# Performance work log

Hardware: AMD Instinct MI355X
Metric: run time of the kernel (lower is better)

Reference implementation:

```python
import jax, jax.numpy as jnp
import numpy as np


def _gcn_conv(x, edge_index, edge_weight, W, b, n_nodes):
    # PyG GCNConv with normalize=True: add self-loops (weight 1), symmetric norm,
    # transform then aggregate: out[col] += norm * (x @ W)[row], plus bias.
    row = jnp.concatenate([edge_index[0], jnp.arange(n_nodes)])
    col = jnp.concatenate([edge_index[1], jnp.arange(n_nodes)])
    w = jnp.concatenate([edge_weight, jnp.ones((n_nodes,), x.dtype)])
    deg = jax.ops.segment_sum(w, col, num_segments=n_nodes)
    dinv = jnp.where(deg > 0, jax.lax.rsqrt(jnp.maximum(deg, 1e-12)), 0.0)
    norm = dinv[row] * w * dinv[col]            # [E+N]
    h = x @ W                                   # [N, out]
    msg = h[row] * norm[:, None]                # [E+N, out]
    out = jax.ops.segment_sum(msg, col, num_segments=n_nodes)
    return out + b


def setup_inputs() -> dict:
    key = jax.random.key(0)
    ks = jax.random.split(key, 6)
    N, E, F_IN, H, C = 50000, 800000, 512, 128, 40
    features = jax.random.normal(ks[0], (N, F_IN), jnp.float32)
    edge_index = jax.random.randint(ks[1], (2, E), 0, N, jnp.int64)
    edge_weight = jax.random.uniform(ks[2], (E,), jnp.float32)
    W1 = jax.random.normal(ks[3], (F_IN, H), jnp.float32) * 0.05
    b1 = jnp.zeros((H,), jnp.float32)
    W2 = jax.random.normal(ks[4], (H, C), jnp.float32) * 0.05
    b2 = jnp.zeros((C,), jnp.float32)
    return {"features": features, "edge_index": edge_index, "edge_weight": edge_weight,
            "W1": W1, "b1": b1, "W2": W2, "b2": b2}


def reference(features, edge_index, edge_weight, W1, b1, W2, b2):
    n_nodes = features.shape[0]
    x = _gcn_conv(features, edge_index, edge_weight, W1, b1, n_nodes)
    x = jax.nn.relu(x)
    # F.dropout(training=self.training): identity in eval mode
    x = _gcn_conv(x, edge_index, edge_weight, W2, b2, n_nodes)
    return jax.nn.log_softmax(x, axis=1)
```

## Files before the change

kernel.cpp:

```cpp
#include <hip/hip_runtime.h>
#include <math.h>

#define FIN  512
#define HDIM 128
#define CDIM 40
#define CPAD 48
#define CAP  64

typedef __attribute__((ext_vector_type(8))) short shortx8;
typedef __attribute__((ext_vector_type(4))) float f32x4;
typedef __attribute__((ext_vector_type(2))) float floatx2;

__device__ inline unsigned short f2bf(float x) {
    unsigned u = __builtin_bit_cast(unsigned, x);
    unsigned r = u + 0x7fffu + ((u >> 16) & 1u);
    return (unsigned short)(r >> 16);
}
__device__ inline float bfu(unsigned short v) { return __builtin_bit_cast(float, (unsigned)v << 16); }
__device__ inline float bfhi(unsigned u) { return __builtin_bit_cast(float, u & 0xffff0000u); }
__device__ inline unsigned char f2fp8(float x) {
    return (unsigned char)(__builtin_amdgcn_cvt_pk_fp8_f32(x, x, 0, false) & 0xff);
}
__device__ inline floatx2 fp8x2_dec(unsigned short v) {
    return __builtin_amdgcn_cvt_pk_f32_fp8((int)(unsigned)v, false);
}
__device__ inline int cur_cnt(unsigned long long p) { return min((int)(p >> 40), CAP); }
__device__ inline float cur_dinv(unsigned long long p) {
    return rsqrtf(1.0f + (float)(p & ((1ULL << 40) - 1)) * 2.3283064365386963e-10f);
}

#define PREPB 280
__global__ void k_fill(const int* __restrict__ row, const int* __restrict__ col,
                       const float* __restrict__ w,
                       unsigned long long* __restrict__ cursor,
                       unsigned* __restrict__ bkt, int E, int eblocks,
                       const float* __restrict__ W1, const float* __restrict__ W2,
                       unsigned short* __restrict__ W1T, unsigned short* __restrict__ W2T) {
    if ((int)blockIdx.x >= eblocks) {
        const int i = ((int)blockIdx.x - eblocks) * 256 + (int)threadIdx.x;
        if (i < FIN * HDIM) {
            const int k = i >> 7, nn = i & 127;
            W1T[nn * FIN + k] = f2bf(W1[i]);
        } else {
            const int j = i - FIN * HDIM;
            const int nn = j >> 7, k = j & 127;
            W2T[j] = (nn < CDIM) ? f2bf(W2[k * CDIM + nn]) : (unsigned short)0;
        }
        return;
    }
    const int e = blockIdx.x * blockDim.x + threadIdx.x;
    if (e >= E) return;
    const int c = col[e];
    const float we = w[e];
    const unsigned long long wfix = (unsigned long long)(we * 4294967296.0f);
    const unsigned long long old = atomicAdd(&cursor[c], (1ULL << 40) | wfix);
    const int p = (int)(old >> 40);
    const unsigned wb = (__builtin_bit_cast(unsigned, we) + 0x8000u) >> 16;
    if (p < CAP) bkt[(size_t)c * CAP + p] = (wb << 16) | (unsigned)row[e];
}

#define G1_LDA 72
__global__ __launch_bounds__(256) void k_gemm1(const float* __restrict__ A,
                                               const unsigned short* __restrict__ W1T,
                                               const unsigned long long* __restrict__ cursor,
                                               unsigned char* __restrict__ h1f8, int M) {
    __shared__ short As[128 * G1_LDA];
    __shared__ short Bs[128 * G1_LDA];
    const int tid  = threadIdx.x;
    const int wave = tid >> 6;
    const int lane = tid & 63;
    const int quad = lane >> 4;
    const int mr   = lane & 15;
    const int m0w  = (wave & 1) * 64;
    const int n0w  = (wave >> 1) * 64;
    const int m0b  = blockIdx.x * 128;

    const int srow = tid >> 1;
    const int spart = tid & 1;

    f32x4 acc[4][4];
#pragma unroll
    for (int i = 0; i < 4; i++)
#pragma unroll
        for (int j = 0; j < 4; j++) acc[i][j] = (f32x4)0.f;

    const int grow = m0b + srow;
    const bool arow_ok = grow < M;
    const float* ap = A + (size_t)grow * FIN + spart * 32;
    const unsigned short* bp = W1T + (size_t)srow * FIN + spart * 32;

    for (int k0 = 0; k0 < FIN; k0 += 64) {
#pragma unroll
        for (int i = 0; i < 4; i++) {
            float4 v0 = make_float4(0.f, 0.f, 0.f, 0.f), v1 = v0;
            if (arow_ok) {
                v0 = *(const float4*)(ap + k0 + i * 8);
                v1 = *(const float4*)(ap + k0 + i * 8 + 4);
            }
            shortx8 pk;
            pk[0] = (short)f2bf(v0.x); pk[1] = (short)f2bf(v0.y);
            pk[2] = (short)f2bf(v0.z); pk[3] = (short)f2bf(v0.w);
            pk[4] = (short)f2bf(v1.x); pk[5] = (short)f2bf(v1.y);
            pk[6] = (short)f2bf(v1.z); pk[7] = (short)f2bf(v1.w);
            *(shortx8*)&As[srow * G1_LDA + spart * 32 + i * 8] = pk;
        }
#pragma unroll
        for (int i = 0; i < 4; i++)
            *(shortx8*)&Bs[srow * G1_LDA + spart * 32 + i * 8] =
                *(const shortx8*)(bp + k0 + i * 8);
        __syncthreads();

#pragma unroll
        for (int kk = 0; kk < 2; kk++) {
            shortx8 af[4], bfr[4];
#pragma unroll
            for (int mt = 0; mt < 4; mt++)
                af[mt] = *(shortx8*)&As[(m0w + mt * 16 + mr) * G1_LDA + kk * 32 + quad * 8];
#pragma unroll
            for (int nt = 0; nt < 4; nt++)
                bfr[nt] = *(shortx8*)&Bs[(n0w + nt * 16 + mr) * G1_LDA + kk * 32 + quad * 8];
#pragma unroll
            for (int mt = 0; mt < 4; mt++)
#pragma unroll
                for (int nt = 0; nt < 4; nt++)
                    acc[mt][nt] = __builtin_amdgcn_mfma_f32_16x16x32_bf16(
                        af[mt], bfr[nt], acc[mt][nt], 0, 0, 0);
        }
        __syncthreads();
    }
#pragma unroll
    for (int mt = 0; mt < 4; mt++)
#pragma unroll
        for (int r = 0; r < 4; r++) {
            const int om = m0b + m0w + mt * 16 + quad * 4 + r;
            if (om < M) {
                const float dv = cur_dinv(cursor[om]);
#pragma unroll
                for (int nt = 0; nt < 4; nt++)
                    h1f8[(size_t)om * HDIM + n0w + nt * 16 + mr] = f2fp8(dv * acc[mt][nt][r]);
            }
        }
}

#define W2LD 130
__global__ __launch_bounds__(256) void k_g1g2(
    const unsigned long long* __restrict__ cursor, const unsigned* __restrict__ bkt,
    const unsigned char* __restrict__ h1f8,
    const float* __restrict__ b1,
    const unsigned short* __restrict__ W2T,
    unsigned short* __restrict__ h2, int n_nodes) {
    __shared__ unsigned short W2s[CPAD * W2LD];
    __shared__ unsigned short Xs[4 * 128];
    const int tid  = threadIdx.x;
    const int wave = tid >> 6;
    const int lane = tid & 63;
    const int loff = lane * 2;

    for (int i = tid; i < CPAD * (HDIM / 8); i += 256) {
        const int r = i >> 4, j = (i & 15) * 8;
        *(shortx8*)&W2s[r * W2LD + j] = *(const shortx8*)(W2T + r * HDIM + j);
    }
    __syncthreads();

    const int node = blockIdx.x * 4 + wave;
    if (node >= n_nodes) return;
    const unsigned long long cp = cursor[node];
    const int cnt = cur_cnt(cp);
    const float dl = cur_dinv(cp);
    const char* bb = (const char*)bkt + (unsigned)node * (CAP * 4u);
    float a0 = 0.f, a1 = 0.f, c0 = 0.f, c1 = 0.f;
    int s = 0;
    for (; s + 8 <= cnt; s += 8) {
        const uint4 qa = *(const uint4*)(bb + (unsigned)s * 4u);
        const uint4 qb = *(const uint4*)(bb + (unsigned)s * 4u + 16u);
        const unsigned o0 = (qa.x & 0xffffu) * 128u + (unsigned)loff;
        const unsigned o1 = (qa.y & 0xffffu) * 128u + (unsigned)loff;
        const unsigned o2 = (qa.z & 0xffffu) * 128u + (unsigned)loff;
        const unsigned o3 = (qa.w & 0xffffu) * 128u + (unsigned)loff;
        const unsigned o4 = (qb.x & 0xffffu) * 128u + (unsigned)loff;
        const unsigned o5 = (qb.y & 0xffffu) * 128u + (unsigned)loff;
        const unsigned o6 = (qb.z & 0xffffu) * 128u + (unsigned)loff;
        const unsigned o7 = (qb.w & 0xffffu) * 128u + (unsigned)loff;
        const unsigned short v0 = *(const unsigned short*)(h1f8 + o0);
        const unsigned short v1 = *(const unsigned short*)(h1f8 + o1);
        const unsigned short v2 = *(const unsigned short*)(h1f8 + o2);
        const unsigned short v3 = *(const unsigned short*)(h1f8 + o3);
        const unsigned short v4 = *(const unsigned short*)(h1f8 + o4);
        const unsigned short v5 = *(const unsigned short*)(h1f8 + o5);
        const unsigned short v6 = *(const unsigned short*)(h1f8 + o6);
        const unsigned short v7 = *(const unsigned short*)(h1f8 + o7);
        const floatx2 f0 = fp8x2_dec(v0), f1 = fp8x2_dec(v1), f2 = fp8x2_dec(v2), f3 = fp8x2_dec(v3);
        const floatx2 f4 = fp8x2_dec(v4), f5 = fp8x2_dec(v5), f6 = fp8x2_dec(v6), f7 = fp8x2_dec(v7);
        a0 += bfhi(qa.x) * f0.x + bfhi(qa.y) * f1.x + bfhi(qa.z) * f2.x + bfhi(qa.w) * f3.x;
        a1 += bfhi(qa.x) * f0.y + bfhi(qa.y) * f1.y + bfhi(qa.z) * f2.y + bfhi(qa.w) * f3.y;
        c0 += bfhi(qb.x) * f4.x + bfhi(qb.y) * f5.x + bfhi(qb.z) * f6.x + bfhi(qb.w) * f7.x;
        c1 += bfhi(qb.x) * f4.y + bfhi(qb.y) * f5.y + bfhi(qb.z) * f6.y + bfhi(qb.w) * f7.y;
    }
    for (; s + 4 <= cnt; s += 4) {
        const uint4 qa = *(const uint4*)(bb + (unsigned)s * 4u);
        const unsigned o0 = (qa.x & 0xffffu) * 128u + (unsigned)loff;
        const unsigned o1 = (qa.y & 0xffffu) * 128u + (unsigned)loff;
        const unsigned o2 = (qa.z & 0xffffu) * 128u + (unsigned)loff;
        const unsigned o3 = (qa.w & 0xffffu) * 128u + (unsigned)loff;
        const unsigned short v0 = *(const unsigned short*)(h1f8 + o0);
        const unsigned short v1 = *(const unsigned short*)(h1f8 + o1);
        const unsigned short v2 = *(const unsigned short*)(h1f8 + o2);
        const unsigned short v3 = *(const unsigned short*)(h1f8 + o3);
        const floatx2 f0 = fp8x2_dec(v0), f1 = fp8x2_dec(v1), f2 = fp8x2_dec(v2), f3 = fp8x2_dec(v3);
        a0 += bfhi(qa.x) * f0.x + bfhi(qa.y) * f1.x + bfhi(qa.z) * f2.x + bfhi(qa.w) * f3.x;
        a1 += bfhi(qa.x) * f0.y + bfhi(qa.y) * f1.y + bfhi(qa.z) * f2.y + bfhi(qa.w) * f3.y;
    }
    for (; s < cnt; s++) {
        const unsigned p = *(const unsigned*)(bb + (unsigned)s * 4u);
        const unsigned short v = *(const unsigned short*)(h1f8 + (p & 0xffffu) * 128u + (unsigned)loff);
        const floatx2 f = fp8x2_dec(v);
        a0 += bfhi(p) * f.x;
        a1 += bfhi(p) * f.y;
    }
    a0 += c0; a1 += c1;
    const unsigned short vs = *(const unsigned short*)(h1f8 + (unsigned)node * 128u + (unsigned)loff);
    const floatx2 fs = fp8x2_dec(vs);
    a0 = fmaxf(dl * (a0 + fs.x) + b1[loff], 0.f);
    a1 = fmaxf(dl * (a1 + fs.y) + b1[loff + 1], 0.f);
    *(unsigned*)&Xs[wave * 128 + loff] = (unsigned)f2bf(a0) | ((unsigned)f2bf(a1) << 16);

    const int quad = lane >> 4;
    const int mr   = lane & 15;
    f32x4 acc2[3];
#pragma unroll
    for (int nt = 0; nt < 3; nt++) acc2[nt] = (f32x4)0.f;
#pragma unroll
    for (int kc = 0; kc < 4; kc++) {
        shortx8 af = (shortx8)0;
        if (mr == 0) af = *(const shortx8*)&Xs[wave * 128 + kc * 32 + quad * 8];
#pragma unroll
        for (int nt = 0; nt < 3; nt++) {
            const shortx8 bfr = *(const shortx8*)&W2s[(nt * 16 + mr) * W2LD + kc * 32 + quad * 8];
            acc2[nt] = __builtin_amdgcn_mfma_f32_16x16x32_bf16(af, bfr, acc2[nt], 0, 0, 0);
        }
    }
    if (lane < 16) {
        h2[(size_t)node * 32 + lane]      = f2bf(dl * acc2[0][0]);
        h2[(size_t)node * 32 + 16 + lane] = f2bf(dl * acc2[1][0]);
        if (lane < 8)
            h2[(size_t)n_nodes * 32 + (size_t)node * 8 + lane] = f2bf(dl * acc2[2][0]);
    }
}

__global__ __launch_bounds__(256) void k_gather2(
    const unsigned long long* __restrict__ cursor, const unsigned* __restrict__ bkt,
    const unsigned short* __restrict__ h2,
    const float* __restrict__ b2,
    float* __restrict__ out, int n_nodes) {
    const int node = blockIdx.x * 4 + (threadIdx.x >> 6);
    const int lane = threadIdx.x & 63;
    if (node >= n_nodes) return;
    const bool act = lane < CDIM;
    const unsigned long long cp = cursor[node];
    const int cnt = cur_cnt(cp);
    const float dl = cur_dinv(cp);
    const char* bb = (const char*)bkt + (unsigned)node * (CAP * 4u);
    const char* h2c = (const char*)h2;
    const unsigned strB = (lane < 32) ? 64u : 16u;
    const unsigned cb   = (lane < 32) ? (unsigned)lane * 2u
                                      : (unsigned)n_nodes * 64u + (unsigned)(lane - 32) * 2u;
    float acc = 0.f, accb = 0.f;
    int s = 0;
    for (; s + 4 <= cnt; s += 4) {
        const uint4 q = *(const uint4*)(bb + (unsigned)s * 4u);
        if (act) {
            const unsigned short u0 = *(const unsigned short*)(h2c + (q.x & 0xffffu) * strB + cb);
            const unsigned short u1 = *(const unsigned short*)(h2c + (q.y & 0xffffu) * strB + cb);
            const unsigned short u2 = *(const unsigned short*)(h2c + (q.z & 0xffffu) * strB + cb);
            const unsigned short u3 = *(const unsigned short*)(h2c + (q.w & 0xffffu) * strB + cb);
            acc  += bfhi(q.x) * bfu(u0) + bfhi(q.y) * bfu(u1);
            accb += bfhi(q.z) * bfu(u2) + bfhi(q.w) * bfu(u3);
        }
    }
    for (; s < cnt; s++) {
        const unsigned p = *(const unsigned*)(bb + (unsigned)s * 4u);
        if (act) acc += bfhi(p) * bfu(*(const unsigned short*)(h2c + (p & 0xffffu) * strB + cb));
    }
    acc += accb;
    if (act) {
        const unsigned short us = *(const unsigned short*)(h2c + (unsigned)node * strB + cb);
        acc = dl * (acc + bfu(us)) + b2[lane];
    }
    float m = act ? acc : -INFINITY;
#pragma unroll
    for (int off = 32; off; off >>= 1) m = fmaxf(m, __shfl_xor(m, off));
    float se = act ? expf(acc - m) : 0.f;
#pragma unroll
    for (int off = 32; off; off >>= 1) se += __shfl_xor(se, off);
    if (act) out[(size_t)node * CDIM + lane] = acc - m - logf(se);
}

extern "C" void kernel_launch(void* const* d_in, const int* in_sizes, int n_in,
                              void* d_out, int out_size, void* d_ws, size_t ws_size,
                              hipStream_t stream) {
    const float* features = (const float*)d_in[0];
    const int*   eidx     = (const int*)d_in[1];
    const float* ew       = (const float*)d_in[2];
    const float* W1       = (const float*)d_in[3];
    const float* b1       = (const float*)d_in[4];
    const float* W2       = (const float*)d_in[5];
    const float* b2       = (const float*)d_in[6];
    float* out = (float*)d_out;

    const int Nn = in_sizes[0] / FIN;
    const int E  = in_sizes[2];
    const int* row = eidx;
    const int* col = eidx + E;

    char* ws = (char*)d_ws;
    size_t off = 0;
    auto alloc = [&](size_t bytes) { void* p = ws + off; off += (bytes + 255) & ~(size_t)255; return p; };
    unsigned long long* cursor = (unsigned long long*)alloc((size_t)Nn * 8);
    unsigned* bkt          = (unsigned*)alloc((size_t)Nn * CAP * 4);
    unsigned short* W1T    = (unsigned short*)alloc((size_t)FIN * HDIM * 2);
    unsigned short* W2T    = (unsigned short*)alloc((size_t)CPAD * HDIM * 2);
    unsigned char*  h1f8   = (unsigned char*) alloc((size_t)Nn * HDIM);
    unsigned short* h2     = (unsigned short*)alloc((size_t)Nn * 40 * 2);

    const int eblocks = (E + 255) / 256;

    hipMemsetAsync(cursor, 0, (size_t)Nn * 8, stream);
    k_fill<<<eblocks + PREPB, 256, 0, stream>>>(row, col, ew, cursor, bkt, E, eblocks,
                                                W1, W2, W1T, W2T);
    k_gemm1<<<(Nn + 127) / 128, 256, 0, stream>>>(features, W1T, cursor, h1f8, Nn);
    k_g1g2<<<(Nn + 3) / 4, 256, 0, stream>>>(cursor, bkt, h1f8, b1, W2T, h2, Nn);
    k_gather2<<<(Nn + 3) / 4, 256, 0, stream>>>(cursor, bkt, h2, b2, out, Nn);
}
```

Measured before the change: 309.3 us.

## Overlap edge bucketing with GEMM1 and move source dinv scaling into gather

New measurement: 287.8 us. 7.0% less time.

```diff
diff --git a/kernel.cpp b/kernel.cpp
--- a/kernel.cpp
+++ b/kernel.cpp
@@ -24,20 +24,14 @@
 __device__ inline floatx2 fp8x2_dec(unsigned short v) {
     return __builtin_amdgcn_cvt_pk_f32_fp8((int)(unsigned)v, false);
 }
-__device__ inline int cur_cnt(unsigned long long p) { return min((int)(p >> 40), CAP); }
-__device__ inline float cur_dinv(unsigned long long p) {
-    return rsqrtf(1.0f + (float)(p & ((1ULL << 40) - 1)) * 2.3283064365386963e-10f);
-}
 
 #define PREPB 280
-__global__ void k_fill(const int* __restrict__ row, const int* __restrict__ col,
-                       const float* __restrict__ w,
-                       unsigned long long* __restrict__ cursor,
-                       unsigned* __restrict__ bkt, int E, int eblocks,
-                       const float* __restrict__ W1, const float* __restrict__ W2,
-                       unsigned short* __restrict__ W1T, unsigned short* __restrict__ W2T) {
-    if ((int)blockIdx.x >= eblocks) {
-        const int i = ((int)blockIdx.x - eblocks) * 256 + (int)threadIdx.x;
+__global__ void k_prep(const float* __restrict__ W1, const float* __restrict__ W2,
+                       unsigned short* __restrict__ W1T, unsigned short* __restrict__ W2T,
+                       unsigned long long* __restrict__ cursor, int n) {
+    const int b = blockIdx.x;
+    if (b < PREPB) {
+        const int i = b * 256 + (int)threadIdx.x;
         if (i < FIN * HDIM) {
             const int k = i >> 7, nn = i & 127;
             W1T[nn * FIN + k] = f2bf(W1[i]);
@@ -46,27 +40,36 @@
             const int nn = j >> 7, k = j & 127;
             W2T[j] = (nn < CDIM) ? f2bf(W2[k * CDIM + nn]) : (unsigned short)0;
         }
-        return;
-    }
-    const int e = blockIdx.x * blockDim.x + threadIdx.x;
-    if (e >= E) return;
-    const int c = col[e];
-    const float we = w[e];
-    const unsigned long long wfix = (unsigned long long)(we * 4294967296.0f);
-    const unsigned long long old = atomicAdd(&cursor[c], (1ULL << 40) | wfix);
-    const int p = (int)(old >> 40);
-    const unsigned wb = (__builtin_bit_cast(unsigned, we) + 0x8000u) >> 16;
-    if (p < CAP) bkt[(size_t)c * CAP + p] = (wb << 16) | (unsigned)row[e];
+    } else {
+        const int i = (b - PREPB) * 256 + (int)threadIdx.x;
+        if (i < n) cursor[i] = 0ULL;
+    }
 }
 
 #define G1_LDA 72
-__global__ __launch_bounds__(256) void k_gemm1(const float* __restrict__ A,
-                                               const unsigned short* __restrict__ W1T,
-                                               const unsigned long long* __restrict__ cursor,
-                                               unsigned char* __restrict__ h1f8, int M) {
+__global__ __launch_bounds__(256) void k_fillg1(
+    const float* __restrict__ A, const unsigned short* __restrict__ W1T,
+    unsigned char* __restrict__ h1f8, int M, int g1b,
+    const int* __restrict__ row, const int* __restrict__ col,
+    const float* __restrict__ w,
+    unsigned long long* __restrict__ cursor, unsigned* __restrict__ bkt, int E) {
     __shared__ short As[128 * G1_LDA];
     __shared__ short Bs[128 * G1_LDA];
-    const int tid  = threadIdx.x;
+    const int tid = threadIdx.x;
+
+    if ((int)blockIdx.x >= g1b) {
+        const int e = ((int)blockIdx.x - g1b) * 256 + tid;
+        if (e >= E) return;
+        const int c = col[e];
+        const float we = w[e];
+        const unsigned long long wfix = (unsigned long long)(we * 4294967296.0f);
+        const unsigned long long old = atomicAdd(&cursor[c], (1ULL << 40) | wfix);
+        const int p = (int)(old >> 40);
+        const unsigned wb = (__builtin_bit_cast(unsigned, we) + 0x8000u) >> 16;
+        if (p < CAP) bkt[(size_t)c * CAP + p] = (wb << 16) | (unsigned)row[e];
+        return;
+    }
+
     const int wave = tid >> 6;
     const int lane = tid & 63;
     const int quad = lane >> 4;
@@ -134,17 +137,27 @@
         for (int r = 0; r < 4; r++) {
             const int om = m0b + m0w + mt * 16 + quad * 4 + r;
             if (om < M) {
-                const float dv = cur_dinv(cursor[om]);
 #pragma unroll
                 for (int nt = 0; nt < 4; nt++)
-                    h1f8[(size_t)om * HDIM + n0w + nt * 16 + mr] = f2fp8(dv * acc[mt][nt][r]);
+                    h1f8[(size_t)om * HDIM + n0w + nt * 16 + mr] = f2fp8(acc[mt][nt][r]);
             }
         }
+}
+
+__global__ void k_dinv(const unsigned long long* __restrict__ cursor,
+                       int* __restrict__ cnt, float* __restrict__ dinv, int n) {
+    const int i = blockIdx.x * 256 + threadIdx.x;
+    if (i < n) {
+        const unsigned long long p = cursor[i];
+        cnt[i] = min((int)(p >> 40), CAP);
+        dinv[i] = rsqrtf(1.0f + (float)(p & ((1ULL << 40) - 1)) * 2.3283064365386963e-10f);
+    }
 }
 
 #define W2LD 130
 __global__ __launch_bounds__(256) void k_g1g2(
-    const unsigned long long* __restrict__ cursor, const unsigned* __restrict__ bkt,
+    const int* __restrict__ cnt_arr, const float* __restrict__ dinv,
+    const unsigned* __restrict__ bkt,
     const unsigned char* __restrict__ h1f8,
     const float* __restrict__ b1,
     const unsigned short* __restrict__ W2T,
@@ -164,64 +177,64 @@
 
     const int node = blockIdx.x * 4 + wave;
     if (node >= n_nodes) return;
-    const unsigned long long cp = cursor[node];
-    const int cnt = cur_cnt(cp);
-    const float dl = cur_dinv(cp);
+    const int cnt = cnt_arr[node];
+    const float dl = dinv[node];
     const char* bb = (const char*)bkt + (unsigned)node * (CAP * 4u);
     float a0 = 0.f, a1 = 0.f, c0 = 0.f, c1 = 0.f;
     int s = 0;
     for (; s + 8 <= cnt; s += 8) {
         const uint4 qa = *(const uint4*)(bb + (unsigned)s * 4u);
         const uint4 qb = *(const uint4*)(bb + (unsigned)s * 4u + 16u);
-        const unsigned o0 = (qa.x & 0xffffu) * 128u + (unsigned)loff;
-        const unsigned o1 = (qa.y & 0xffffu) * 128u + (unsigned)loff;
-        const unsigned o2 = (qa.z & 0xffffu) * 128u + (unsigned)loff;
-        const unsigned o3 = (qa.w & 0xffffu) * 128u + (unsigned)loff;
-        const unsigned o4 = (qb.x & 0xffffu) * 128u + (unsigned)loff;
-        const unsigned o5 = (qb.y & 0xffffu) * 128u + (unsigned)loff;
-        const unsigned o6 = (qb.z & 0xffffu) * 128u + (unsigned)loff;
-        const unsigned o7 = (qb.w & 0xffffu) * 128u + (unsigned)loff;
-        const unsigned short v0 = *(const unsigned short*)(h1f8 + o0);
-        const unsigned short v1 = *(const unsigned short*)(h1f8 + o1);
-        const unsigned short v2 = *(const unsigned short*)(h1f8 + o2);
-        const unsigned short v3 = *(const unsigned short*)(h1f8 + o3);
-        const unsigned short v4 = *(const unsigned short*)(h1f8 + o4);
-        const unsigned short v5 = *(const unsigned short*)(h1f8 + o5);
-        const unsigned short v6 = *(const unsigned short*)(h1f8 + o6);
-        const unsigned short v7 = *(const unsigned short*)(h1f8 + o7);
+        const float w0 = bfhi(qa.x) * dinv[qa.x & 0xffffu];
+        const float w1 = bfhi(qa.y) * dinv[qa.y & 0xffffu];
+        const float w2 = bfhi(qa.z) * dinv[qa.z & 0xffffu];
+        const float w3 = bfhi(qa.w) * dinv[qa.w & 0xffffu];
+        const float w4 = bfhi(qb.x) * dinv[qb.x & 0xffffu];
+        const float w5 = bfhi(qb.y) * dinv[qb.y & 0xffffu];
+        const float w6 = bfhi(qb.z) * dinv[qb.z & 0xffffu];
+        const float w7 = bfhi(qb.w) * dinv[qb.w & 0xffffu];
+        const unsigned short v0 = *(const unsigned short*)(h1f8 + (qa.x & 0xffffu) * 128u + (unsigned)loff);
+        const unsigned short v1 = *(const unsigned short*)(h1f8 + (qa.y & 0xffffu) * 128u + (unsigned)loff);
+        const unsigned short v2 = *(const unsigned short*)(h1f8 + (qa.z & 0xffffu) * 128u + (unsigned)loff);
+        const unsigned short v3 = *(const unsigned short*)(h1f8 + (qa.w & 0xffffu) * 128u + (unsigned)loff);
+        const unsigned short v4 = *(const unsigned short*)(h1f8 + (qb.x & 0xffffu) * 128u + (unsigned)loff);
+        const unsigned short v5 = *(const unsigned short*)(h1f8 + (qb.y & 0xffffu) * 128u + (unsigned)loff);
+        const unsigned short v6 = *(const unsigned short*)(h1f8 + (qb.z & 0xffffu) * 128u + (unsigned)loff);
+        const unsigned short v7 = *(const unsigned short*)(h1f8 + (qb.w & 0xffffu) * 128u + (unsigned)loff);
         const floatx2 f0 = fp8x2_dec(v0), f1 = fp8x2_dec(v1), f2 = fp8x2_dec(v2), f3 = fp8x2_dec(v3);
         const floatx2 f4 = fp8x2_dec(v4), f5 = fp8x2_dec(v5), f6 = fp8x2_dec(v6), f7 = fp8x2_dec(v7);
-        a0 += bfhi(qa.x) * f0.x + bfhi(qa.y) * f1.x + bfhi(qa.z) * f2.x + bfhi(qa.w) * f3.x;
-        a1 += bfhi(qa.x) * f0.y + bfhi(qa.y) * f1.y + bfhi(qa.z) * f2.y + bfhi(qa.w) * f3.y;
-        c0 += bfhi(qb.x) * f4.x + bfhi(qb.y) * f5.x + bfhi(qb.z) * f6.x + bfhi(qb.w) * f7.x;
-        c1 += bfhi(qb.x) * f4.y + bfhi(qb.y) * f5.y + bfhi(qb.z) * f6.y + bfhi(qb.w) * f7.y;
+        a0 += w0 * f0.x + w1 * f1.x + w2 * f2.x + w3 * f3.x;
+        a1 += w0 * f0.y + w1 * f1.y + w2 * f2.y + w3 * f3.y;
+        c0 += w4 * f4.x + w5 * f5.x + w6 * f6.x + w7 * f7.x;
+        c1 += w4 * f4.y + w5 * f5.y + w6 * f6.y + w7 * f7.y;
     }
     for (; s + 4 <= cnt; s += 4) {
         const uint4 qa = *(const uint4*)(bb + (unsigned)s * 4u);
-        const unsigned o0 = (qa.x & 0xffffu) * 128u + (unsigned)loff;
-        const unsigned o1 = (qa.y & 0xffffu) * 128u + (unsigned)loff;
-        const unsigned o2 = (qa.z & 0xffffu) * 128u + (unsigned)loff;
-        const unsigned o3 = (qa.w & 0xffffu) * 128u + (unsigned)loff;
-        const unsigned short v0 = *(const unsigned short*)(h1f8 + o0);
-        const unsigned short v1 = *(const unsigned short*)(h1f8 + o1);
-        const unsigned short v2 = *(const unsigned short*)(h1f8 + o2);
-        const unsigned short v3 = *(const unsigned short*)(h1f8 + o3);
+        const float w0 = bfhi(qa.x) * dinv[qa.x & 0xffffu];
+        const float w1 = bfhi(qa.y) * dinv[qa.y & 0xffffu];
+        const float w2 = bfhi(qa.z) * dinv[qa.z & 0xffffu];
+        const float w3 = bfhi(qa.w) * dinv[qa.w & 0xffffu];
+        const unsigned short v0 = *(const unsigned short*)(h1f8 + (qa.x & 0xffffu) * 128u + (unsigned)loff);
+        const unsigned short v1 = *(const unsigned short*)(h1f8 + (qa.y & 0xffffu) * 128u + (unsigned)loff);
+        const unsigned short v2 = *(const unsigned short*)(h1f8 + (qa.z & 0xffffu) * 128u + (unsigned)loff);
+        const unsigned short v3 = *(const unsigned short*)(h1f8 + (qa.w & 0xffffu) * 128u + (unsigned)loff);
         const floatx2 f0 = fp8x2_dec(v0), f1 = fp8x2_dec(v1), f2 = fp8x2_dec(v2), f3 = fp8x2_dec(v3);
-        a0 += bfhi(qa.x) * f0.x + bfhi(qa.y) * f1.x + bfhi(qa.z) * f2.x + bfhi(qa.w) * f3.x;
-        a1 += bfhi(qa.x) * f0.y + bfhi(qa.y) * f1.y + bfhi(qa.z) * f2.y + bfhi(qa.w) * f3.y;
+        a0 += w0 * f0.x + w1 * f1.x + w2 * f2.x + w3 * f3.x;
+        a1 += w0 * f0.y + w1 * f1.y + w2 * f2.y + w3 * f3.y;
     }
     for (; s < cnt; s++) {
         const unsigned p = *(const unsigned*)(bb + (unsigned)s * 4u);
+        const float w0 = bfhi(p) * dinv[p & 0xffffu];
         const unsigned short v = *(const unsigned short*)(h1f8 + (p & 0xffffu) * 128u + (unsigned)loff);
         const floatx2 f = fp8x2_dec(v);
-        a0 += bfhi(p) * f.x;
-        a1 += bfhi(p) * f.y;
+        a0 += w0 * f.x;
+        a1 += w0 * f.y;
     }
     a0 += c0; a1 += c1;
     const unsigned short vs = *(const unsigned short*)(h1f8 + (unsigned)node * 128u + (unsigned)loff);
     const floatx2 fs = fp8x2_dec(vs);
-    a0 = fmaxf(dl * (a0 + fs.x) + b1[loff], 0.f);
-    a1 = fmaxf(dl * (a1 + fs.y) + b1[loff + 1], 0.f);
+    a0 = fmaxf(dl * (a0 + dl * fs.x) + b1[loff], 0.f);
+    a1 = fmaxf(dl * (a1 + dl * fs.y) + b1[loff + 1], 0.f);
     *(unsigned*)&Xs[wave * 128 + loff] = (unsigned)f2bf(a0) | ((unsigned)f2bf(a1) << 16);
 
     const int quad = lane >> 4;
@@ -248,7 +261,8 @@
 }
 
 __global__ __launch_bounds__(256) void k_gather2(
-    const unsigned long long* __restrict__ cursor, const unsigned* __restrict__ bkt,
+    const int* __restrict__ cnt_arr, const float* __restrict__ dinv,
+    const unsigned* __restrict__ bkt,
     const unsigned short* __restrict__ h2,
     const float* __restrict__ b2,
     float* __restrict__ out, int n_nodes) {
@@ -256,9 +270,8 @@
     const int lane = threadIdx.x & 63;
     if (node >= n_nodes) return;
     const bool act = lane < CDIM;
-    const unsigned long long cp = cursor[node];
-    const int cnt = cur_cnt(cp);
-    const float dl = cur_dinv(cp);
+    const int cnt = cnt_arr[node];
+    const float dl = dinv[node];
     const char* bb = (const char*)bkt + (unsigned)node * (CAP * 4u);
     const char* h2c = (const char*)h2;
     const unsigned strB = (lane < 32) ? 64u : 16u;
@@ -316,6 +329,8 @@
     size_t off = 0;
     auto alloc = [&](size_t bytes) { void* p = ws + off; off += (bytes + 255) & ~(size_t)255; return p; };
     unsigned long long* cursor = (unsigned long long*)alloc((size_t)Nn * 8);
+    int*      cnt          = (int*)     alloc((size_t)Nn * 4);
+    float*    dinv         = (float*)   alloc((size_t)Nn * 4);
     unsigned* bkt          = (unsigned*)alloc((size_t)Nn * CAP * 4);
     unsigned short* W1T    = (unsigned short*)alloc((size_t)FIN * HDIM * 2);
     unsigned short* W2T    = (unsigned short*)alloc((size_t)CPAD * HDIM * 2);
@@ -323,11 +338,12 @@
     unsigned short* h2     = (unsigned short*)alloc((size_t)Nn * 40 * 2);
 
     const int eblocks = (E + 255) / 256;
-
-    hipMemsetAsync(cursor, 0, (size_t)Nn * 8, stream);
-    k_fill<<<eblocks + PREPB, 256, 0, stream>>>(row, col, ew, cursor, bkt, E, eblocks,
-                                                W1, W2, W1T, W2T);
-    k_gemm1<<<(Nn + 127) / 128, 256, 0, stream>>>(features, W1T, cursor, h1f8, Nn);
-    k_g1g2<<<(Nn + 3) / 4, 256, 0, stream>>>(cursor, bkt, h1f8, b1, W2T, h2, Nn);
-    k_gather2<<<(Nn + 3) / 4, 256, 0, stream>>>(cursor, bkt, h2, b2, out, Nn);
-}
+    const int g1b = (Nn + 127) / 128;
+
+    k_prep<<<PREPB + (Nn + 255) / 256, 256, 0, stream>>>(W1, W2, W1T, W2T, cursor, Nn);
+    k_fillg1<<<g1b + eblocks, 256, 0, stream>>>(features, W1T, h1f8, Nn, g1b,
+                                                row, col, ew, cursor, bkt, E);
+    k_dinv<<<(Nn + 255) / 256, 256, 0, stream>>>(cursor, cnt, dinv, Nn);
+    k_g1g2<<<(Nn + 3) / 4, 256, 0, stream>>>(cnt, dinv, bkt, h1f8, b1, W2T, h2, Nn);
+    k_gather2<<<(Nn + 3) / 4, 256, 0, stream>>>(cnt, dinv, bkt, h2, b2, out, Nn);
+}
```
